# Performance work log

Measured on AMD Instinct MI355X. Metric: run time of the kernel, lower is better.

Reference implementation:

```python
import jax, jax.numpy as jnp
import numpy as np

H, C = 4, 32
NT, NDAT, NDEV = 50000, 20000, 4
EDT, EVT, ETT = 800000, 200000, 400000


def _gat_conv(xs, xd, src, dst, ea, Ws, Wd, We, As, Ad, Ae, b, n_dst, concat):
    # linear projections -> [N, H, C]
    hs = (xs @ Ws).reshape(-1, H, C)
    hd = (xd @ Wd).reshape(-1, H, C)
    he = (ea @ We).reshape(-1, H, C)
    # per-edge attention logits [E, H]
    al = (hs * As).sum(-1)[src] + (hd * Ad).sum(-1)[dst] + (he * Ae).sum(-1)
    al = jax.nn.leaky_relu(al, 0.2)
    # segment softmax over incoming edges of each dst node
    amax = jax.ops.segment_max(al, dst, num_segments=n_dst)
    amax = jnp.where(jnp.isfinite(amax), amax, 0.0)
    ex = jnp.exp(al - amax[dst])
    den = jax.ops.segment_sum(ex, dst, num_segments=n_dst)
    w = ex / (den[dst] + 1e-16)
    # weighted scatter-add of source messages
    out = jax.ops.segment_sum(hs[src] * w[..., None], dst, num_segments=n_dst)
    out = out.reshape(n_dst, H * C) if concat else out.mean(axis=1)
    return out + b


def _add_self_loops_mean(src, dst, ea, n):
    # PyG add_self_loops(fill_value='mean'): loop edge_attr = mean of incoming edge_attr per node
    cnt = jax.ops.segment_sum(jnp.ones(dst.shape, ea.dtype), dst, num_segments=n)
    ea_mean = jax.ops.segment_sum(ea, dst, num_segments=n) / jnp.maximum(cnt, 1.0)[:, None]
    loops = jnp.arange(n, dtype=src.dtype)
    return (jnp.concatenate([src, loops]), jnp.concatenate([dst, loops]),
            jnp.concatenate([ea, ea_mean], axis=0))


def setup_inputs() -> dict:
    key = jax.random.key(0)
    ks = iter(jax.random.split(key, 40))
    nrm = lambda shape, fan: jax.random.normal(next(ks), shape, jnp.float32) / np.sqrt(fan)
    inp = {}
    inp['x_data'] = jax.random.normal(next(ks), (NDAT, 8), jnp.float32)
    inp['x_tasks'] = jax.random.normal(next(ks), (NT, 16), jnp.float32)
    inp['x_dev'] = jax.random.normal(next(ks), (NDEV, 8), jnp.float32)
    inp['ei_dt'] = jnp.stack([jax.random.randint(next(ks), (EDT,), 0, NDAT),
                              jax.random.randint(next(ks), (EDT,), 0, NT)]).astype(jnp.int32)
    inp['ea_dt'] = jax.random.normal(next(ks), (EDT, 8), jnp.float32)
    inp['ei_vt'] = jnp.stack([jax.random.randint(next(ks), (EVT,), 0, NDEV),
                              jax.random.randint(next(ks), (EVT,), 0, NT)]).astype(jnp.int32)
    inp['ea_vt'] = jax.random.normal(next(ks), (EVT, 6), jnp.float32)
    inp['ei_tt'] = jnp.stack([jax.random.randint(next(ks), (ETT,), 0, NT),
                              jax.random.randint(next(ks), (ETT,), 0, NT)]).astype(jnp.int32)
    inp['ea_tt'] = jax.random.normal(next(ks), (ETT, 4), jnp.float32)
    # conv1: (data -> tasks), concat=True
    inp['Ws1'] = nrm((8, H * C), 8); inp['Wd1'] = nrm((16, H * C), 16); inp['We1'] = nrm((8, H * C), 8)
    inp['As1'] = nrm((H, C), C); inp['Ad1'] = nrm((H, C), C); inp['Ae1'] = nrm((H, C), C)
    inp['b1'] = jnp.zeros((H * C,), jnp.float32)
    # conv2: (devices -> tasks), concat=True
    inp['Ws2'] = nrm((8, H * C), 8); inp['Wd2'] = nrm((16, H * C), 16); inp['We2'] = nrm((6, H * C), 6)
    inp['As2'] = nrm((H, C), C); inp['Ad2'] = nrm((H, C), C); inp['Ae2'] = nrm((H, C), C)
    inp['b2'] = jnp.zeros((H * C,), jnp.float32)
    # conv3: tasks -> tasks, single lin (256 -> H*C), concat=False, self loops
    inp['W3'] = nrm((2 * H * C, H * C), 2 * H * C); inp['We3'] = nrm((4, H * C), 4)
    inp['As3'] = nrm((H, C), C); inp['Ad3'] = nrm((H, C), C); inp['Ae3'] = nrm((H, C), C)
    inp['b3'] = jnp.zeros((C,), jnp.float32)
    return inp


def reference(x_data, x_tasks, x_dev, ei_dt, ea_dt, ei_vt, ea_vt, ei_tt, ea_tt,
              Ws1, Wd1, We1, As1, Ad1, Ae1, b1,
              Ws2, Wd2, We2, As2, Ad2, Ae2, b2,
              W3, We3, As3, Ad3, Ae3, b3):
    t_data = jax.nn.relu(_gat_conv(x_data, x_tasks, ei_dt[0], ei_dt[1], ea_dt,
                                   Ws1, Wd1, We1, As1, Ad1, Ae1, b1, NT, True))
    t_dev = jax.nn.relu(_gat_conv(x_dev, x_tasks, ei_vt[0], ei_vt[1], ea_vt,
                                  Ws2, Wd2, We2, As2, Ad2, Ae2, b2, NT, True))
    tasks = jnp.concatenate([t_data, t_dev], axis=1)  # [NT, 256]
    src, dst, ea = _add_self_loops_mean(ei_tt[0], ei_tt[1], ea_tt, NT)
    x = _gat_conv(tasks, tasks, src, dst, ea, W3, W3, We3, As3, Ad3, Ae3, b3, NT, False)
    x = jax.nn.relu(x)
    # dropout(p=0.5) is identity in eval mode
    return x
```

## Files before the change

kernel.cpp:

```cpp
#include <hip/hip_runtime.h>
#include <math.h>

static const int NT = 50000, NDAT = 20000, NDEV = 4;
static const int EDT = 800000, EVT = 200000, ETT = 400000;

static const int SCAN_TILE = 2048, SCAN_NB = 25;

static const int HT   = EDT + EVT + ETT;
static const int IN_A = HT + NDAT * 128;
static const int IN_B = IN_A + NDAT * 4;
static const int IN_C = IN_B + NT * 4;
static const int IN_D = IN_C + NDEV * 128;
static const int IN_E = IN_D + NDEV * 4;
static const int IN_F = IN_E + 256 * 128;
static const int FRONT_N = IN_F;

static const size_t OFF_TASKS = 0;
static const size_t OFF_HS    = 12800000;
static const size_t OFF_RANK  = OFF_HS;
static const size_t OFF_HSB1  = OFF_HS + 1400000;
static const size_t OFF_REC1  = OFF_HS + 2680000;
static const size_t OFF_HSB3  = OFF_HS;
static const size_t OFF_REC2  = 19200000;
static const size_t OFF_REC3  = 20000000;
static const size_t OFF_DEG   = 23200000;
static const size_t OFF_RP    = 23350000;
static const size_t OFF_AS1   = 23500004;
static const size_t OFF_AD1   = 23580004;
static const size_t OFF_AD2   = 23780004;
static const size_t OFF_HS2   = 23980004;
static const size_t OFF_AS2   = 23980516;
static const size_t OFF_QS1   = 23980532;
static const size_t OFF_QD1   = 23980564;
static const size_t OFF_P1    = 23980628;
static const size_t OFF_QS2   = 23980660;
static const size_t OFF_QD2   = 23980692;
static const size_t OFF_P2    = 23980756;
static const size_t OFF_P3    = 23980780;
static const size_t OFF_BSUM  = 23980796;
static const size_t OFF_W3HT  = 23980924;
static const size_t OFF_W3LT  = 23997308;
static const size_t WS_TOTAL  = 24013692;

typedef short v8s __attribute__((ext_vector_type(8)));
typedef float v4f __attribute__((ext_vector_type(4)));

__device__ __forceinline__ float lrelu(float a) { return a > 0.f ? a : 0.2f * a; }
__device__ __forceinline__ unsigned short f2bf(float x) {
    unsigned int u = __float_as_uint(x);
    return (unsigned short)((u + 0x7FFFu + ((u >> 16) & 1u)) >> 16);
}
__device__ __forceinline__ float bf2f(unsigned short h) {
    return __uint_as_float(((unsigned int)h) << 16);
}
__device__ __forceinline__ float bfsel(unsigned int lo01, unsigned int lo23, int h) {
    unsigned int word = (h < 2) ? lo01 : lo23;
    return bf2f((unsigned short)((h & 1) ? (word >> 16) : (word & 0xFFFFu)));
}
__device__ __forceinline__ void cvt_split(const float4& A, const float4& B, v8s& hi, v8s& lo) {
    union { unsigned short u[8]; v8s v; } H, L;
    float f[8] = {A.x, A.y, A.z, A.w, B.x, B.y, B.z, B.w};
    #pragma unroll
    for (int i = 0; i < 8; ++i) {
        unsigned short h = f2bf(f[i]);
        H.u[i] = h;
        L.u[i] = f2bf(f[i] - bf2f(h));
    }
    hi = H.v; lo = L.v;
}

__global__ void k_proj_small(const float* Ws1, const float* As1,
                             const float* Wd1, const float* Ad1,
                             const float* We1, const float* Ae1,
                             const float* Ws2, const float* As2,
                             const float* Wd2, const float* Ad2,
                             const float* We2, const float* Ae2,
                             const float* We3, const float* Ae3,
                             float* Qs1, float* Qd1, float* P1,
                             float* Qs2, float* Qd2, float* P2, float* P3) {
    int t = threadIdx.x;
    const float *W, *A; float* O; int u;
    if      (t < 32)  { W = Ws1; A = As1; O = Qs1; u = t; }
    else if (t < 96)  { W = Wd1; A = Ad1; O = Qd1; u = t - 32; }
    else if (t < 128) { W = We1; A = Ae1; O = P1;  u = t - 96; }
    else if (t < 160) { W = Ws2; A = As2; O = Qs2; u = t - 128; }
    else if (t < 224) { W = Wd2; A = Ad2; O = Qd2; u = t - 160; }
    else if (t < 248) { W = We2; A = Ae2; O = P2;  u = t - 224; }
    else if (t < 264) { W = We3; A = Ae3; O = P3;  u = t - 248; }
    else return;
    int k = u >> 2, h = u & 3;
    float acc = 0.f;
    for (int c = 0; c < 32; ++c) acc += W[k * 128 + h * 32 + c] * A[h * 32 + c];
    O[k * 4 + h] = acc;
}

__global__ __launch_bounds__(256) void k_front(const float* __restrict__ x_data,
                                               const float* __restrict__ Ws1,
                                               unsigned short* __restrict__ hsb1,
                                               const float* __restrict__ Qs1,
                                               float* __restrict__ as1,
                                               const float* __restrict__ x_tasks,
                                               const float* __restrict__ Qd1,
                                               const float* __restrict__ Qd2,
                                               float* __restrict__ ad1, float* __restrict__ ad2,
                                               const float* __restrict__ x_dev,
                                               const float* __restrict__ Ws2,
                                               float* __restrict__ hs2,
                                               const float* __restrict__ Qs2,
                                               float* __restrict__ as2,
                                               const float* __restrict__ W3,
                                               unsigned short* __restrict__ w3hT,
                                               unsigned short* __restrict__ w3lT,
                                               const int* __restrict__ dt,
                                               const int* __restrict__ vt,
                                               const int* __restrict__ tt,
                                               int* __restrict__ deg,
                                               int* __restrict__ rank) {
    int idx = blockIdx.x * blockDim.x + threadIdx.x;
    if (idx < HT) {
        if (idx < EDT) {
            int d = dt[EDT + idx];
            int r = atomicAdd(&deg[d], 1);
            rank[idx] = (r << 16) | d;
        } else if (idx < EDT + EVT) {
            int d = vt[EVT + (idx - EDT)];
            int r = atomicAdd(&deg[NT + d], 1);
            rank[idx] = (r << 16) | d;
        } else {
            int d = tt[ETT + (idx - EDT - EVT)];
            int r = atomicAdd(&deg[2 * NT + d], 1);
            rank[idx] = (r << 16) | d;
        }
    } else if (idx < IN_A) {
        int i = idx - HT;
        int n = i >> 7, j = i & 127;
        float acc = 0.f;
        #pragma unroll
        for (int k = 0; k < 8; ++k) acc += x_data[n * 8 + k] * Ws1[k * 128 + j];
        hsb1[i] = f2bf(acc);
    } else if (idx < IN_B) {
        int i = idx - IN_A;
        int n = i >> 2, h = i & 3;
        float acc = 0.f;
        #pragma unroll
        for (int k = 0; k < 8; ++k) acc += x_data[n * 8 + k] * Qs1[k * 4 + h];
        as1[i] = acc;
    } else if (idx < IN_C) {
        int i = idx - IN_B;
        int n = i >> 2, h = i & 3;
        float a = 0.f, b = 0.f;
        #pragma unroll
        for (int k = 0; k < 16; ++k) {
            float v = x_tasks[n * 16 + k];
            a += v * Qd1[k * 4 + h];
            b += v * Qd2[k * 4 + h];
        }
        ad1[i] = a; ad2[i] = b;
    } else if (idx < IN_D) {
        int i = idx - IN_C;
        int n = i >> 7, j = i & 127;
        float acc = 0.f;
        #pragma unroll
        for (int k = 0; k < 8; ++k) acc += x_dev[n * 8 + k] * Ws2[k * 128 + j];
        hs2[i] = acc;
    } else if (idx < IN_E) {
        int i = idx - IN_D;
        int n = i >> 2, h = i & 3;
        float acc = 0.f;
        #pragma unroll
        for (int k = 0; k < 8; ++k) acc += x_dev[n * 8 + k] * Qs2[k * 4 + h];
        as2[i] = acc;
    } else if (idx < IN_F) {
        int i = idx - IN_E;
        int k = i >> 7, n = i & 127;
        float x = W3[i];
        unsigned short h = f2bf(x);
        w3hT[n * 256 + k] = h;
        w3lT[n * 256 + k] = f2bf(x - bf2f(h));
    }
}

__global__ __launch_bounds__(256) void k_scan_part(const int* __restrict__ deg,
                                                   int* __restrict__ bsum) {
    int b = blockIdx.x;
    int g = b / SCAN_NB, t = b % SCAN_NB;
    int base = t * SCAN_TILE + threadIdx.x * 8;
    const int* dg = deg + (size_t)g * NT;
    int s = 0;
    if (base + 8 <= NT) {
        int4 a = *reinterpret_cast<const int4*>(dg + base);
        int4 c = *reinterpret_cast<const int4*>(dg + base + 4);
        s = a.x + a.y + a.z + a.w + c.x + c.y + c.z + c.w;
    } else {
        for (int i = 0; i < 8; ++i) if (base + i < NT) s += dg[base + i];
    }
    __shared__ int red[256];
    red[threadIdx.x] = s;
    __syncthreads();
    for (int off = 128; off > 0; off >>= 1) {
        if (threadIdx.x < off) red[threadIdx.x] += red[threadIdx.x + off];
        __syncthreads();
    }
    if (threadIdx.x == 0) bsum[b] = red[0];
}

__global__ __launch_bounds__(256) void k_scan_final(const int* __restrict__ deg,
                                                    const int* __restrict__ bsum,
                                                    int* __restrict__ rp) {
    int b = blockIdx.x;
    int g = b / SCAN_NB, t = b % SCAN_NB;
    int tid = threadIdx.x;
    int base = t * SCAN_TILE + tid * 8;
    const int* dg = deg + (size_t)g * NT;
    int* rpg = rp + (size_t)g * (NT + 1);
    int v[8];
    int s = 0;
    if (base + 8 <= NT) {
        int4 a = *reinterpret_cast<const int4*>(dg + base);
        int4 c = *reinterpret_cast<const int4*>(dg + base + 4);
        v[0] = a.x; v[1] = a.y; v[2] = a.z; v[3] = a.w;
        v[4] = c.x; v[5] = c.y; v[6] = c.z; v[7] = c.w;
        s = v[0] + v[1] + v[2] + v[3] + v[4] + v[5] + v[6] + v[7];
    } else {
        #pragma unroll
        for (int i = 0; i < 8; ++i) {
            v[i] = (base + i < NT) ? dg[base + i] : 0;
            s += v[i];
        }
    }
    __shared__ int sums[256];
    sums[tid] = s;
    __syncthreads();
    for (int off = 1; off < 256; off <<= 1) {
        int x = (tid >= off) ? sums[tid - off] : 0;
        __syncthreads();
        sums[tid] += x;
        __syncthreads();
    }
    int toff = 0;
    for (int t2 = 0; t2 < t; ++t2) toff += bsum[g * SCAN_NB + t2];
    int run = toff + (tid ? sums[tid - 1] : 0);
    #pragma unroll
    for (int i = 0; i < 8; ++i) {
        int idx = base + i;
        if (idx < NT) {
            rpg[idx] = run; run += v[i];
            if (idx == NT - 1) rpg[NT] = run;
        }
    }
}

__global__ void k_permute_w(const int* __restrict__ dt, const int* __restrict__ vt,
                            const int* __restrict__ tt, const int* __restrict__ rank,
                            const int* __restrict__ rp,
                            const float* __restrict__ as1, const float* __restrict__ ad1,
                            const float* __restrict__ P1, const float* __restrict__ ea1,
                            const float* __restrict__ as2, const float* __restrict__ ad2,
                            const float* __restrict__ P2, const float* __restrict__ ea2,
                            const float* __restrict__ P3, const float* __restrict__ ea3,
                            uint4* __restrict__ rec1, uint4* __restrict__ rec2,
                            uint4* __restrict__ rec3) {
    int e = blockIdx.x * blockDim.x + threadIdx.x;
    if (e < EDT) {
        int rk = rank[e];
        int d = rk & 0xFFFF;
        int s = dt[e];
        int slot = rp[d] + (rk >> 16);
        float l[4];
        #pragma unroll
        for (int h = 0; h < 4; ++h) l[h] = as1[s * 4 + h] + ad1[d * 4 + h];
        float4 A = *reinterpret_cast<const float4*>(&ea1[(size_t)e * 8]);
        float4 B = *reinterpret_cast<const float4*>(&ea1[(size_t)e * 8 + 4]);
        float ev[8] = {A.x, A.y, A.z, A.w, B.x, B.y, B.z, B.w};
        #pragma unroll
        for (int k = 0; k < 8; ++k)
            #pragma unroll
            for (int h = 0; h < 4; ++h) l[h] += ev[k] * P1[k * 4 + h];
        unsigned int w01 = (unsigned int)f2bf(expf(lrelu(l[0])))
                         | ((unsigned int)f2bf(expf(lrelu(l[1]))) << 16);
        unsigned int w23 = (unsigned int)f2bf(expf(lrelu(l[2])))
                         | ((unsigned int)f2bf(expf(lrelu(l[3]))) << 16);
        rec1[slot] = make_uint4(w01, w23, (unsigned int)s, 0u);
    } else if (e < EDT + EVT) {
        int ee = e - EDT;
        int rk = rank[e];
        int d = rk & 0xFFFF;
        int s = vt[ee];
        int slot = rp[(NT + 1) + d] + (rk >> 16);
        float l[4];
        #pragma unroll
        for (int h = 0; h < 4; ++h) l[h] = as2[s * 4 + h] + ad2[d * 4 + h];
        float2 a = *reinterpret_cast<const float2*>(&ea2[(size_t)ee * 6]);
        float2 b = *reinterpret_cast<const float2*>(&ea2[(size_t)ee * 6 + 2]);
        float2 c = *reinterpret_cast<const float2*>(&ea2[(size_t)ee * 6 + 4]);
        float ev[6] = {a.x, a.y, b.x, b.y, c.x, c.y};
        #pragma unroll
        for (int k = 0; k < 6; ++k)
            #pragma unroll
            for (int h = 0; h < 4; ++h) l[h] += ev[k] * P2[k * 4 + h];
        unsigned int w01 = (unsigned int)f2bf(expf(lrelu(l[0])))
                         | ((unsigned int)f2bf(expf(lrelu(l[1]))) << 16);
        unsigned int w23 = (unsigned int)f2bf(expf(lrelu(l[2])))
                         | ((unsigned int)f2bf(expf(lrelu(l[3]))) << 16);
        rec2[slot] = make_uint4(w01, w23, (unsigned int)s, 0u);
    } else if (e < EDT + EVT + ETT) {
        int ee = e - EDT - EVT;
        int rk = rank[e];
        int d = rk & 0xFFFF;
        int s = tt[ee];
        int slot = rp[2 * (NT + 1) + d] + (rk >> 16);
        float4 q = *reinterpret_cast<const float4*>(&ea3[(size_t)ee * 4]);
        float ae[4];
        #pragma unroll
        for (int h = 0; h < 4; ++h)
            ae[h] = q.x * P3[h] + q.y * P3[4 + h] + q.z * P3[8 + h] + q.w * P3[12 + h];
        unsigned int a01 = (unsigned int)f2bf(ae[0]) | ((unsigned int)f2bf(ae[1]) << 16);
        unsigned int a23 = (unsigned int)f2bf(ae[2]) | ((unsigned int)f2bf(ae[3]) << 16);
        rec3[slot] = make_uint4((unsigned int)s, a01, a23, 0u);
    }
}

__global__ __launch_bounds__(256) void k_gather12(const int* __restrict__ rp1,
                                                  const uint4* __restrict__ rec1,
                                                  const unsigned short* __restrict__ hsb,
                                                  const float* __restrict__ b1,
                                                  const int* __restrict__ rp2,
                                                  const uint4* __restrict__ rec2,
                                                  const float* __restrict__ hs2,
                                                  const float* __restrict__ b2,
                                                  float* __restrict__ tasks) {
    int tid = threadIdx.x;
    int lane = tid & 31;
    int h = lane >> 3;
    if (blockIdx.x < NT / 8) {
        int d = blockIdx.x * 8 + (tid >> 5);
        int c0 = (lane & 7) * 4;
        int i0 = rp1[d], i1 = rp1[d + 1];
        float a0 = 0.f, a1 = 0.f, a2 = 0.f, a3 = 0.f, den = 0.f;
        int i = i0;
        for (; i + 4 <= i1; i += 4) {
            uint4 r0 = rec1[i], r1 = rec1[i + 1], r2 = rec1[i + 2], r3 = rec1[i + 3];
            float w0 = bfsel(r0.x, r0.y, h);
            float w1 = bfsel(r1.x, r1.y, h);
            float w2 = bfsel(r2.x, r2.y, h);
            float w3 = bfsel(r3.x, r3.y, h);
            ushort4 m0 = *reinterpret_cast<const ushort4*>(&hsb[(size_t)r0.z * 128 + h * 32 + c0]);
            ushort4 m1 = *reinterpret_cast<const ushort4*>(&hsb[(size_t)r1.z * 128 + h * 32 + c0]);
            ushort4 m2 = *reinterpret_cast<const ushort4*>(&hsb[(size_t)r2.z * 128 + h * 32 + c0]);
            ushort4 m3 = *reinterpret_cast<const ushort4*>(&hsb[(size_t)r3.z * 128 + h * 32 + c0]);
            a0 += w0 * bf2f(m0.x) + w1 * bf2f(m1.x) + w2 * bf2f(m2.x) + w3 * bf2f(m3.x);
            a1 += w0 * bf2f(m0.y) + w1 * bf2f(m1.y) + w2 * bf2f(m2.y) + w3 * bf2f(m3.y);
            a2 += w0 * bf2f(m0.z) + w1 * bf2f(m1.z) + w2 * bf2f(m2.z) + w3 * bf2f(m3.z);
            a3 += w0 * bf2f(m0.w) + w1 * bf2f(m1.w) + w2 * bf2f(m2.w) + w3 * bf2f(m3.w);
            den += w0 + w1 + w2 + w3;
        }
        for (; i < i1; ++i) {
            uint4 r = rec1[i];
            float w = bfsel(r.x, r.y, h);
            ushort4 m = *reinterpret_cast<const ushort4*>(&hsb[(size_t)r.z * 128 + h * 32 + c0]);
            a0 += w * bf2f(m.x); a1 += w * bf2f(m.y);
            a2 += w * bf2f(m.z); a3 += w * bf2f(m.w);
            den += w;
        }
        int j0 = h * 32 + c0;
        float4 b4 = *reinterpret_cast<const float4*>(&b1[j0]);
        float r = 1.f / (den + 1e-16f);
        float4 o = make_float4(fmaxf(a0 * r + b4.x, 0.f), fmaxf(a1 * r + b4.y, 0.f),
                               fmaxf(a2 * r + b4.z, 0.f), fmaxf(a3 * r + b4.w, 0.f));
        *reinterpret_cast<float4*>(&tasks[(size_t)d * 256 + j0]) = o;
    } else {
        int d = (blockIdx.x - NT / 8) * 8 + (tid >> 5);
        int i0 = rp2[d], i1 = rp2[d + 1];
        float ax = 0.f, ay = 0.f, az = 0.f, aw = 0.f, den = 0.f;
        int i = i0;
        for (; i + 4 <= i1; i += 4) {
            uint4 r0 = rec2[i], r1 = rec2[i + 1], r2 = rec2[i + 2], r3 = rec2[i + 3];
            float w0 = bfsel(r0.x, r0.y, h);
            float w1 = bfsel(r1.x, r1.y, h);
            float w2 = bfsel(r2.x, r2.y, h);
            float w3 = bfsel(r3.x, r3.y, h);
            float4 v0 = *reinterpret_cast<const float4*>(&hs2[r0.z * 128 + lane * 4]);
            float4 v1 = *reinterpret_cast<const float4*>(&hs2[r1.z * 128 + lane * 4]);
            float4 v2 = *reinterpret_cast<const float4*>(&hs2[r2.z * 128 + lane * 4]);
            float4 v3 = *reinterpret_cast<const float4*>(&hs2[r3.z * 128 + lane * 4]);
            ax += v0.x * w0 + v1.x * w1 + v2.x * w2 + v3.x * w3;
            ay += v0.y * w0 + v1.y * w1 + v2.y * w2 + v3.y * w3;
            az += v0.z * w0 + v1.z * w1 + v2.z * w2 + v3.z * w3;
            aw += v0.w * w0 + v1.w * w1 + v2.w * w2 + v3.w * w3;
            den += w0 + w1 + w2 + w3;
        }
        for (; i < i1; ++i) {
            uint4 r4 = rec2[i];
            float w = bfsel(r4.x, r4.y, h);
            float4 v = *reinterpret_cast<const float4*>(&hs2[r4.z * 128 + lane * 4]);
            ax += v.x * w; ay += v.y * w; az += v.z * w; aw += v.w * w;
            den += w;
        }
        float4 b4 = *reinterpret_cast<const float4*>(&b2[lane * 4]);
        float r = 1.f / (den + 1e-16f);
        float4 o = make_float4(fmaxf(ax * r + b4.x, 0.f), fmaxf(ay * r + b4.y, 0.f),
                               fmaxf(az * r + b4.z, 0.f), fmaxf(aw * r + b4.w, 0.f));
        *reinterpret_cast<float4*>(&tasks[(size_t)d * 256 + 128 + lane * 4]) = o;
    }
}

__global__ __launch_bounds__(256) void k_gather_c3(const int* __restrict__ rp,
                                                   const uint4* __restrict__ rec,
                                                   const float* __restrict__ as3,
                                                   const float* __restrict__ ad3,
                                                   const unsigned short* __restrict__ hsb,
                                                   const float* __restrict__ b3,
                                                   float* __restrict__ out) {
    int tid = threadIdx.x;
    int d = blockIdx.x * 8 + (tid >> 5);
    int lane = tid & 31;
    int h = lane >> 3;
    int c0 = (lane & 7) * 4;
    float adv = ad3[d * 4 + h];
    int i0 = rp[d], i1 = rp[d + 1];
    float a0 = 0.f, a1 = 0.f, a2 = 0.f, a3 = 0.f, den = 0.f, aes = 0.f;
    int i = i0;
    for (; i + 4 <= i1; i += 4) {
        uint4 r0 = rec[i], r1 = rec[i + 1], r2 = rec[i + 2], r3 = rec[i + 3];
        float s0 = as3[(size_t)r0.x * 4 + h], s1 = as3[(size_t)r1.x * 4 + h];
        float s2 = as3[(size_t)r2.x * 4 + h], s3 = as3[(size_t)r3.x * 4 + h];
        ushort4 m0 = *reinterpret_cast<const ushort4*>(&hsb[(size_t)r0.x * 128 + h * 32 + c0]);
        ushort4 m1 = *reinterpret_cast<const ushort4*>(&hsb[(size_t)r1.x * 128 + h * 32 + c0]);
        ushort4 m2 = *reinterpret_cast<const ushort4*>(&hsb[(size_t)r2.x * 128 + h * 32 + c0]);
        ushort4 m3 = *reinterpret_cast<const ushort4*>(&hsb[(size_t)r3.x * 128 + h * 32 + c0]);
        float ae0 = bfsel(r0.y, r0.z, h);
        float ae1 = bfsel(r1.y, r1.z, h);
        float ae2 = bfsel(r2.y, r2.z, h);
        float ae3 = bfsel(r3.y, r3.z, h);
        float w0 = expf(lrelu(s0 + adv + ae0));
        float w1 = expf(lrelu(s1 + adv + ae1));
        float w2 = expf(lrelu(s2 + adv + ae2));
        float w3 = expf(lrelu(s3 + adv + ae3));
        a0 += w0 * bf2f(m0.x) + w1 * bf2f(m1.x) + w2 * bf2f(m2.x) + w3 * bf2f(m3.x);
        a1 += w0 * bf2f(m0.y) + w1 * bf2f(m1.y) + w2 * bf2f(m2.y) + w3 * bf2f(m3.y);
        a2 += w0 * bf2f(m0.z) + w1 * bf2f(m1.z) + w2 * bf2f(m2.z) + w3 * bf2f(m3.z);
        a3 += w0 * bf2f(m0.w) + w1 * bf2f(m1.w) + w2 * bf2f(m2.w) + w3 * bf2f(m3.w);
        den += w0 + w1 + w2 + w3;
        aes += ae0 + ae1 + ae2 + ae3;
    }
    for (; i < i1; ++i) {
        uint4 r4 = rec[i];
        float s = as3[(size_t)r4.x * 4 + h];
        ushort4 m = *reinterpret_cast<const ushort4*>(&hsb[(size_t)r4.x * 128 + h * 32 + c0]);
        float ae = bfsel(r4.y, r4.z, h);
        float w = expf(lrelu(s + adv + ae));
        a0 += w * bf2f(m.x); a1 += w * bf2f(m.y);
        a2 += w * bf2f(m.z); a3 += w * bf2f(m.w);
        den += w; aes += ae;
    }
    float cnt = (float)(i1 - i0);
    float mloop = aes / fmaxf(cnt, 1.f);
    float exl = expf(lrelu(as3[(size_t)d * 4 + h] + adv + mloop));
    ushort4 md = *reinterpret_cast<const ushort4*>(&hsb[(size_t)d * 128 + h * 32 + c0]);
    float rden = 1.f / (den + exl + 1e-16f);
    float p0 = (a0 + exl * bf2f(md.x)) * rden;
    float p1 = (a1 + exl * bf2f(md.y)) * rden;
    float p2 = (a2 + exl * bf2f(md.z)) * rden;
    float p3 = (a3 + exl * bf2f(md.w)) * rden;
    p0 += __shfl_xor(p0, 8, 32); p0 += __shfl_xor(p0, 16, 32);
    p1 += __shfl_xor(p1, 8, 32); p1 += __shfl_xor(p1, 16, 32);
    p2 += __shfl_xor(p2, 8, 32); p2 += __shfl_xor(p2, 16, 32);
    p3 += __shfl_xor(p3, 8, 32); p3 += __shfl_xor(p3, 16, 32);
    if ((lane >> 3) == 0) {
        float4 o;
        o.x = fmaxf(0.25f * p0 + b3[c0 + 0], 0.f);
        o.y = fmaxf(0.25f * p1 + b3[c0 + 1], 0.f);
        o.z = fmaxf(0.25f * p2 + b3[c0 + 2], 0.f);
        o.w = fmaxf(0.25f * p3 + b3[c0 + 3], 0.f);
        *reinterpret_cast<float4*>(&out[(size_t)d * 32 + c0]) = o;
    }
}

__global__ __launch_bounds__(256, 2) void k_gemm_mfma(const float* __restrict__ T,
                                                      const unsigned short* __restrict__ w3hT,
                                                      const unsigned short* __restrict__ w3lT,
                                                      const float* __restrict__ As3,
                                                      const float* __restrict__ Ad3,
                                                      unsigned short* __restrict__ hsb,
                                                      float* __restrict__ as3o,
                                                      float* __restrict__ ad3o) {
    __shared__ uint4 sB[2][2048];
    int tid = threadIdx.x;
    int lane = tid & 63;
    int arow = lane & 15;
    int kgrp = lane >> 4;
    int s0 = blockIdx.x * 8 + (tid >> 6) * 2;
    int ss0 = s0 < 3125 ? s0 : 3124;
    int ss1 = (s0 + 1) < 3125 ? (s0 + 1) : 3124;
    const uint4* w3h4 = reinterpret_cast<const uint4*>(w3hT);
    const uint4* w3l4 = reinterpret_cast<const uint4*>(w3lT);

    v4f acc[2][8];
    #pragma unroll
    for (int sp = 0; sp < 2; ++sp)
        #pragma unroll
        for (int nt = 0; nt < 8; ++nt) acc[sp][nt] = (v4f)0.f;

    #pragma unroll
    for (int kt = 0; kt < 2; ++kt) {
        __syncthreads();
        float4 a0[8], a1[8];
        const float* Ta0 = T + (size_t)(ss0 * 16 + arow) * 256 + kt * 128 + kgrp * 8;
        const float* Ta1 = T + (size_t)(ss1 * 16 + arow) * 256 + kt * 128 + kgrp * 8;
        #pragma unroll
        for (int kc = 0; kc < 4; ++kc) {
            a0[kc * 2]     = *reinterpret_cast<const float4*>(Ta0 + kc * 32);
            a0[kc * 2 + 1] = *reinterpret_cast<const float4*>(Ta0 + kc * 32 + 4);
            a1[kc * 2]     = *reinterpret_cast<const float4*>(Ta1 + kc * 32);
            a1[kc * 2 + 1] = *reinterpret_cast<const float4*>(Ta1 + kc * 32 + 4);
        }
        #pragma unroll
        for (int it = 0; it < 8; ++it) {
            int c = it * 256 + tid;
            int n = c >> 4, ch = c & 15;
            int gi = n * 32 + kt * 16 + ch;
            int li = n * 16 + (ch ^ (n & 7));
            sB[0][li] = w3h4[gi];
            sB[1][li] = w3l4[gi];
        }
        __syncthreads();
        #pragma unroll
        for (int kc = 0; kc < 4; ++kc) {
            v8s ah0, al0, ah1, al1;
            cvt_split(a0[kc * 2], a0[kc * 2 + 1], ah0, al0);
            cvt_split(a1[kc * 2], a1[kc * 2 + 1], ah1, al1);
            #pragma unroll
            for (int nt = 0; nt < 8; ++nt) {
                int col = nt * 16 + arow;
                int ch = kc * 4 + kgrp;
                int li = col * 16 + (ch ^ (col & 7));
                v8s bh = *reinterpret_cast<const v8s*>(&sB[0][li]);
                v8s bl = *reinterpret_cast<const v8s*>(&sB[1][li]);
                acc[0][nt] = __builtin_amdgcn_mfma_f32_16x16x32_bf16(ah0, bh, acc[0][nt], 0, 0, 0);
                acc[0][nt] = __builtin_amdgcn_mfma_f32_16x16x32_bf16(ah0, bl, acc[0][nt], 0, 0, 0);
                acc[0][nt] = __builtin_amdgcn_mfma_f32_16x16x32_bf16(al0, bh, acc[0][nt], 0, 0, 0);
                acc[1][nt] = __builtin_amdgcn_mfma_f32_16x16x32_bf16(ah1, bh, acc[1][nt], 0, 0, 0);
                acc[1][nt] = __builtin_amdgcn_mfma_f32_16x16x32_bf16(ah1, bl, acc[1][nt], 0, 0, 0);
                acc[1][nt] = __builtin_amdgcn_mfma_f32_16x16x32_bf16(al1, bh, acc[1][nt], 0, 0, 0);
            }
        }
    }
    float As3v[8], Ad3v[8];
    #pragma unroll
    for (int nt = 0; nt < 8; ++nt) {
        As3v[nt] = As3[nt * 16 + arow];
        Ad3v[nt] = Ad3[nt * 16 + arow];
    }
    #pragma unroll
    for (int sp = 0; sp < 2; ++sp) {
        int s = s0 + sp;
        if (s >= 3125) continue;
        #pragma unroll
        for (int i = 0; i < 4; ++i) {
            int row = s * 16 + kgrp * 4 + i;
            #pragma unroll
            for (int nt = 0; nt < 8; ++nt)
                hsb[(size_t)row * 128 + nt * 16 + arow] = f2bf(acc[sp][nt][i]);
            #pragma unroll
            for (int h = 0; h < 4; ++h) {
                float pa = acc[sp][2 * h][i] * As3v[2 * h] + acc[sp][2 * h + 1][i] * As3v[2 * h + 1];
                float pb = acc[sp][2 * h][i] * Ad3v[2 * h] + acc[sp][2 * h + 1][i] * Ad3v[2 * h + 1];
                #pragma unroll
                for (int off = 1; off < 16; off <<= 1) {
                    pa += __shfl_xor(pa, off, 64);
                    pb += __shfl_xor(pb, off, 64);
                }
                if (arow == 0) {
                    as3o[row * 4 + h] = pa;
                    ad3o[row * 4 + h] = pb;
                }
            }
        }
    }
}

extern "C" void kernel_launch(void* const* d_in, const int* in_sizes, int n_in,
                              void* d_out, int out_size, void* d_ws, size_t ws_size,
                              hipStream_t stream) {
    const float* x_data  = (const float*)d_in[0];
    const float* x_tasks = (const float*)d_in[1];
    const float* x_dev   = (const float*)d_in[2];
    const int*   ei_dt   = (const int*)d_in[3];
    const float* ea_dt   = (const float*)d_in[4];
    const int*   ei_vt   = (const int*)d_in[5];
    const float* ea_vt   = (const float*)d_in[6];
    const int*   ei_tt   = (const int*)d_in[7];
    const float* ea_tt   = (const float*)d_in[8];
    const float* Ws1 = (const float*)d_in[9];  const float* Wd1 = (const float*)d_in[10];
    const float* We1 = (const float*)d_in[11]; const float* As1 = (const float*)d_in[12];
    const float* Ad1 = (const float*)d_in[13]; const float* Ae1 = (const float*)d_in[14];
    const float* b1  = (const float*)d_in[15];
    const float* Ws2 = (const float*)d_in[16]; const float* Wd2 = (const float*)d_in[17];
    const float* We2 = (const float*)d_in[18]; const float* As2 = (const float*)d_in[19];
    const float* Ad2 = (const float*)d_in[20]; const float* Ae2 = (const float*)d_in[21];
    const float* b2  = (const float*)d_in[22];
    const float* W3  = (const float*)d_in[23]; const float* We3 = (const float*)d_in[24];
    const float* As3 = (const float*)d_in[25]; const float* Ad3 = (const float*)d_in[26];
    const float* Ae3 = (const float*)d_in[27]; const float* b3  = (const float*)d_in[28];

    if (ws_size < WS_TOTAL * sizeof(float)) return;

    float* w = (float*)d_ws;
    float* tasks = w + OFF_TASKS;
    int*   rank  = (int*)(w + OFF_RANK);
    unsigned short* hsb1 = (unsigned short*)(w + OFF_HSB1);
    unsigned short* hsb3 = (unsigned short*)(w + OFF_HSB3);
    uint4* rec1  = (uint4*)(w + OFF_REC1);
    uint4* rec2  = (uint4*)(w + OFF_REC2);
    uint4* rec3  = (uint4*)(w + OFF_REC3);
    int*   deg   = (int*)(w + OFF_DEG);
    int*   rp    = (int*)(w + OFF_RP);
    int*   bsum  = (int*)(w + OFF_BSUM);
    unsigned short* w3hT = (unsigned short*)(w + OFF_W3HT);
    unsigned short* w3lT = (unsigned short*)(w + OFF_W3LT);
    float* as1 = w + OFF_AS1;
    float* ad1 = w + OFF_AD1; float* as3 = w + OFF_AD1;
    float* ad2 = w + OFF_AD2; float* ad3 = w + OFF_AD2;
    float* hs2 = w + OFF_HS2; float* as2 = w + OFF_AS2;
    float* Qs1 = w + OFF_QS1; float* Qd1 = w + OFF_QD1; float* P1 = w + OFF_P1;
    float* Qs2 = w + OFF_QS2; float* Qd2 = w + OFF_QD2; float* P2 = w + OFF_P2;
    float* P3  = w + OFF_P3;
    float* out = (float*)d_out;

    dim3 B(256);
    #define GRID(n) dim3((unsigned)(((n) + 255) / 256))

    hipMemsetAsync(deg, 0, 3 * NT * sizeof(int), stream);
    k_proj_small<<<1, 320, 0, stream>>>(Ws1, As1, Wd1, Ad1, We1, Ae1,
                                        Ws2, As2, Wd2, Ad2, We2, Ae2, We3, Ae3,
                                        Qs1, Qd1, P1, Qs2, Qd2, P2, P3);
    k_front<<<GRID(FRONT_N), B, 0, stream>>>(x_data, Ws1, hsb1, Qs1, as1,
                                             x_tasks, Qd1, Qd2, ad1, ad2,
                                             x_dev, Ws2, hs2, Qs2, as2,
                                             W3, w3hT, w3lT,
                                             ei_dt, ei_vt, ei_tt, deg, rank);
    k_scan_part<<<dim3(3 * SCAN_NB), B, 0, stream>>>(deg, bsum);
    k_scan_final<<<dim3(3 * SCAN_NB), B, 0, stream>>>(deg, bsum, rp);
    k_permute_w<<<GRID(EDT + EVT + ETT), B, 0, stream>>>(ei_dt, ei_vt, ei_tt, rank, rp,
                                                         as1, ad1, P1, ea_dt,
                                                         as2, ad2, P2, ea_vt,
                                                         P3, ea_tt,
                                                         rec1, rec2, rec3);
    k_gather12<<<dim3(2 * (NT / 8)), B, 0, stream>>>(rp, rec1, hsb1, b1,
                                                     rp + (NT + 1), rec2, hs2, b2, tasks);
    k_gemm_mfma<<<dim3(391), dim3(256), 0, stream>>>(tasks, w3hT, w3lT, As3, Ad3,
                                                     hsb3, as3, ad3);
    k_gather_c3<<<dim3(NT / 8), B, 0, stream>>>(rp + 2 * (NT + 1), rec3, as3, ad3,
                                                hsb3, b3, out);
    #undef GRID
}
```

Before: 213.7 us.

## Recompute conv1 source projection on the fly in gather instead of materializing

Stops precomputing the bf16 x_data@Ws1 table (20000x128) in k_front. k_gather12 now keeps each lane's 8x4 slice of Ws1 in registers and rebuilds the message from the 8-float x_data row of every edge. Each edge gathers 32 bytes of raw features instead of a 256-byte projected row, and the front kernel loses 2.56M threads of work. In exchange every edge costs about 32 extra FMAs per lane. Because messages are now computed in fp32 rather than rounded to bf16, precision improves slightly.

```diff
diff --git a/kernel.cpp b/kernel.cpp
--- a/kernel.cpp
+++ b/kernel.cpp
@@ -7,8 +7,7 @@
 static const int SCAN_TILE = 2048, SCAN_NB = 25;
 
 static const int HT   = EDT + EVT + ETT;
-static const int IN_A = HT + NDAT * 128;
-static const int IN_B = IN_A + NDAT * 4;
+static const int IN_B = HT + NDAT * 4;
 static const int IN_C = IN_B + NT * 4;
 static const int IN_D = IN_C + NDEV * 128;
 static const int IN_E = IN_D + NDEV * 4;
@@ -18,7 +17,6 @@
 static const size_t OFF_TASKS = 0;
 static const size_t OFF_HS    = 12800000;
 static const size_t OFF_RANK  = OFF_HS;
-static const size_t OFF_HSB1  = OFF_HS + 1400000;
 static const size_t OFF_REC1  = OFF_HS + 2680000;
 static const size_t OFF_HSB3  = OFF_HS;
 static const size_t OFF_REC2  = 19200000;
@@ -95,8 +93,6 @@
 }
 
 __global__ __launch_bounds__(256) void k_front(const float* __restrict__ x_data,
-                                               const float* __restrict__ Ws1,
-                                               unsigned short* __restrict__ hsb1,
                                                const float* __restrict__ Qs1,
                                                float* __restrict__ as1,
                                                const float* __restrict__ x_tasks,
@@ -131,15 +127,8 @@
             int r = atomicAdd(&deg[2 * NT + d], 1);
             rank[idx] = (r << 16) | d;
         }
-    } else if (idx < IN_A) {
+    } else if (idx < IN_B) {
         int i = idx - HT;
-        int n = i >> 7, j = i & 127;
-        float acc = 0.f;
-        #pragma unroll
-        for (int k = 0; k < 8; ++k) acc += x_data[n * 8 + k] * Ws1[k * 128 + j];
-        hsb1[i] = f2bf(acc);
-    } else if (idx < IN_B) {
-        int i = idx - IN_A;
         int n = i >> 2, h = i & 3;
         float acc = 0.f;
         #pragma unroll
@@ -322,7 +311,8 @@
 
 __global__ __launch_bounds__(256) void k_gather12(const int* __restrict__ rp1,
                                                   const uint4* __restrict__ rec1,
-                                                  const unsigned short* __restrict__ hsb,
+                                                  const float* __restrict__ xd,
+                                                  const float* __restrict__ Ws1,
                                                   const float* __restrict__ b1,
                                                   const int* __restrict__ rp2,
                                                   const uint4* __restrict__ rec2,
@@ -334,7 +324,10 @@
     int h = lane >> 3;
     if (blockIdx.x < NT / 8) {
         int d = blockIdx.x * 8 + (tid >> 5);
-        int c0 = (lane & 7) * 4;
+        float4 Wc[8];
+        #pragma unroll
+        for (int k = 0; k < 8; ++k)
+            Wc[k] = *reinterpret_cast<const float4*>(&Ws1[k * 128 + lane * 4]);
         int i0 = rp1[d], i1 = rp1[d + 1];
         float a0 = 0.f, a1 = 0.f, a2 = 0.f, a3 = 0.f, den = 0.f;
         int i = i0;
@@ -344,25 +337,71 @@
             float w1 = bfsel(r1.x, r1.y, h);
             float w2 = bfsel(r2.x, r2.y, h);
             float w3 = bfsel(r3.x, r3.y, h);
-            ushort4 m0 = *reinterpret_cast<const ushort4*>(&hsb[(size_t)r0.z * 128 + h * 32 + c0]);
-            ushort4 m1 = *reinterpret_cast<const ushort4*>(&hsb[(size_t)r1.z * 128 + h * 32 + c0]);
-            ushort4 m2 = *reinterpret_cast<const ushort4*>(&hsb[(size_t)r2.z * 128 + h * 32 + c0]);
-            ushort4 m3 = *reinterpret_cast<const ushort4*>(&hsb[(size_t)r3.z * 128 + h * 32 + c0]);
-            a0 += w0 * bf2f(m0.x) + w1 * bf2f(m1.x) + w2 * bf2f(m2.x) + w3 * bf2f(m3.x);
-            a1 += w0 * bf2f(m0.y) + w1 * bf2f(m1.y) + w2 * bf2f(m2.y) + w3 * bf2f(m3.y);
-            a2 += w0 * bf2f(m0.z) + w1 * bf2f(m1.z) + w2 * bf2f(m2.z) + w3 * bf2f(m3.z);
-            a3 += w0 * bf2f(m0.w) + w1 * bf2f(m1.w) + w2 * bf2f(m2.w) + w3 * bf2f(m3.w);
+            float4 xa0 = *reinterpret_cast<const float4*>(&xd[(size_t)r0.z * 8]);
+            float4 xb0 = *reinterpret_cast<const float4*>(&xd[(size_t)r0.z * 8 + 4]);
+            float4 xa1 = *reinterpret_cast<const float4*>(&xd[(size_t)r1.z * 8]);
+            float4 xb1 = *reinterpret_cast<const float4*>(&xd[(size_t)r1.z * 8 + 4]);
+            float4 xa2 = *reinterpret_cast<const float4*>(&xd[(size_t)r2.z * 8]);
+            float4 xb2 = *reinterpret_cast<const float4*>(&xd[(size_t)r2.z * 8 + 4]);
+            float4 xa3 = *reinterpret_cast<const float4*>(&xd[(size_t)r3.z * 8]);
+            float4 xb3 = *reinterpret_cast<const float4*>(&xd[(size_t)r3.z * 8 + 4]);
+            float4 m0, m1, m2, m3;
+            m0.x = xa0.x*Wc[0].x + xa0.y*Wc[1].x + xa0.z*Wc[2].x + xa0.w*Wc[3].x
+                 + xb0.x*Wc[4].x + xb0.y*Wc[5].x + xb0.z*Wc[6].x + xb0.w*Wc[7].x;
+            m0.y = xa0.x*Wc[0].y + xa0.y*Wc[1].y + xa0.z*Wc[2].y + xa0.w*Wc[3].y
+                 + xb0.x*Wc[4].y + xb0.y*Wc[5].y + xb0.z*Wc[6].y + xb0.w*Wc[7].y;
+            m0.z = xa0.x*Wc[0].z + xa0.y*Wc[1].z + xa0.z*Wc[2].z + xa0.w*Wc[3].z
+                 + xb0.x*Wc[4].z + xb0.y*Wc[5].z + xb0.z*Wc[6].z + xb0.w*Wc[7].z;
+            m0.w = xa0.x*Wc[0].w + xa0.y*Wc[1].w + xa0.z*Wc[2].w + xa0.w*Wc[3].w
+                 + xb0.x*Wc[4].w + xb0.y*Wc[5].w + xb0.z*Wc[6].w + xb0.w*Wc[7].w;
+            m1.x = xa1.x*Wc[0].x + xa1.y*Wc[1].x + xa1.z*Wc[2].x + xa1.w*Wc[3].x
+                 + xb1.x*Wc[4].x + xb1.y*Wc[5].x + xb1.z*Wc[6].x + xb1.w*Wc[7].x;
+            m1.y = xa1.x*Wc[0].y + xa1.y*Wc[1].y + xa1.z*Wc[2].y + xa1.w*Wc[3].y
+                 + xb1.x*Wc[4].y + xb1.y*Wc[5].y + xb1.z*Wc[6].y + xb1.w*Wc[7].y;
+            m1.z = xa1.x*Wc[0].z + xa1.y*Wc[1].z + xa1.z*Wc[2].z + xa1.w*Wc[3].z
+                 + xb1.x*Wc[4].z + xb1.y*Wc[5].z + xb1.z*Wc[6].z + xb1.w*Wc[7].z;
+            m1.w = xa1.x*Wc[0].w + xa1.y*Wc[1].w + xa1.z*Wc[2].w + xa1.w*Wc[3].w
+                 + xb1.x*Wc[4].w + xb1.y*Wc[5].w + xb1.z*Wc[6].w + xb1.w*Wc[7].w;
+            m2.x = xa2.x*Wc[0].x + xa2.y*Wc[1].x + xa2.z*Wc[2].x + xa2.w*Wc[3].x
+                 + xb2.x*Wc[4].x + xb2.y*Wc[5].x + xb2.z*Wc[6].x + xb2.w*Wc[7].x;
+            m2.y = xa2.x*Wc[0].y + xa2.y*Wc[1].y + xa2.z*Wc[2].y + xa2.w*Wc[3].y
+                 + xb2.x*Wc[4].y + xb2.y*Wc[5].y + xb2.z*Wc[6].y + xb2.w*Wc[7].y;
+            m2.z = xa2.x*Wc[0].z + xa2.y*Wc[1].z + xa2.z*Wc[2].z + xa2.w*Wc[3].z
+                 + xb2.x*Wc[4].z + xb2.y*Wc[5].z + xb2.z*Wc[6].z + xb2.w*Wc[7].z;
+            m2.w = xa2.x*Wc[0].w + xa2.y*Wc[1].w + xa2.z*Wc[2].w + xa2.w*Wc[3].w
+                 + xb2.x*Wc[4].w + xb2.y*Wc[5].w + xb2.z*Wc[6].w + xb2.w*Wc[7].w;
+            m3.x = xa3.x*Wc[0].x + xa3.y*Wc[1].x + xa3.z*Wc[2].x + xa3.w*Wc[3].x
+                 + xb3.x*Wc[4].x + xb3.y*Wc[5].x + xb3.z*Wc[6].x + xb3.w*Wc[7].x;
+            m3.y = xa3.x*Wc[0].y + xa3.y*Wc[1].y + xa3.z*Wc[2].y + xa3.w*Wc[3].y
+                 + xb3.x*Wc[4].y + xb3.y*Wc[5].y + xb3.z*Wc[6].y + xb3.w*Wc[7].y;
+            m3.z = xa3.x*Wc[0].z + xa3.y*Wc[1].z + xa3.z*Wc[2].z + xa3.w*Wc[3].z
+                 + xb3.x*Wc[4].z + xb3.y*Wc[5].z + xb3.z*Wc[6].z + xb3.w*Wc[7].z;
+            m3.w = xa3.x*Wc[0].w + xa3.y*Wc[1].w + xa3.z*Wc[2].w + xa3.w*Wc[3].w
+                 + xb3.x*Wc[4].w + xb3.y*Wc[5].w + xb3.z*Wc[6].w + xb3.w*Wc[7].w;
+            a0 += w0 * m0.x + w1 * m1.x + w2 * m2.x + w3 * m3.x;
+            a1 += w0 * m0.y + w1 * m1.y + w2 * m2.y + w3 * m3.y;
+            a2 += w0 * m0.z + w1 * m1.z + w2 * m2.z + w3 * m3.z;
+            a3 += w0 * m0.w + w1 * m1.w + w2 * m2.w + w3 * m3.w;
             den += w0 + w1 + w2 + w3;
         }
         for (; i < i1; ++i) {
             uint4 r = rec1[i];
             float w = bfsel(r.x, r.y, h);
-            ushort4 m = *reinterpret_cast<const ushort4*>(&hsb[(size_t)r.z * 128 + h * 32 + c0]);
-            a0 += w * bf2f(m.x); a1 += w * bf2f(m.y);
-            a2 += w * bf2f(m.z); a3 += w * bf2f(m.w);
+            float4 xa = *reinterpret_cast<const float4*>(&xd[(size_t)r.z * 8]);
+            float4 xb = *reinterpret_cast<const float4*>(&xd[(size_t)r.z * 8 + 4]);
+            float4 m;
+            m.x = xa.x*Wc[0].x + xa.y*Wc[1].x + xa.z*Wc[2].x + xa.w*Wc[3].x
+                + xb.x*Wc[4].x + xb.y*Wc[5].x + xb.z*Wc[6].x + xb.w*Wc[7].x;
+            m.y = xa.x*Wc[0].y + xa.y*Wc[1].y + xa.z*Wc[2].y + xa.w*Wc[3].y
+                + xb.x*Wc[4].y + xb.y*Wc[5].y + xb.z*Wc[6].y + xb.w*Wc[7].y;
+            m.z = xa.x*Wc[0].z + xa.y*Wc[1].z + xa.z*Wc[2].z + xa.w*Wc[3].z
+                + xb.x*Wc[4].z + xb.y*Wc[5].z + xb.z*Wc[6].z + xb.w*Wc[7].z;
+            m.w = xa.x*Wc[0].w + xa.y*Wc[1].w + xa.z*Wc[2].w + xa.w*Wc[3].w
+                + xb.x*Wc[4].w + xb.y*Wc[5].w + xb.z*Wc[6].w + xb.w*Wc[7].w;
+            a0 += w * m.x; a1 += w * m.y; a2 += w * m.z; a3 += w * m.w;
             den += w;
         }
-        int j0 = h * 32 + c0;
+        int j0 = lane * 4;
         float4 b4 = *reinterpret_cast<const float4*>(&b1[j0]);
         float r = 1.f / (den + 1e-16f);
         float4 o = make_float4(fmaxf(a0 * r + b4.x, 0.f), fmaxf(a1 * r + b4.y, 0.f),
@@ -608,7 +647,6 @@
     float* w = (float*)d_ws;
     float* tasks = w + OFF_TASKS;
     int*   rank  = (int*)(w + OFF_RANK);
-    unsigned short* hsb1 = (unsigned short*)(w + OFF_HSB1);
     unsigned short* hsb3 = (unsigned short*)(w + OFF_HSB3);
     uint4* rec1  = (uint4*)(w + OFF_REC1);
     uint4* rec2  = (uint4*)(w + OFF_REC2);
@@ -634,7 +672,7 @@
     k_proj_small<<<1, 320, 0, stream>>>(Ws1, As1, Wd1, Ad1, We1, Ae1,
                                         Ws2, As2, Wd2, Ad2, We2, Ae2, We3, Ae3,
                                         Qs1, Qd1, P1, Qs2, Qd2, P2, P3);
-    k_front<<<GRID(FRONT_N), B, 0, stream>>>(x_data, Ws1, hsb1, Qs1, as1,
+    k_front<<<GRID(FRONT_N), B, 0, stream>>>(x_data, Qs1, as1,
                                              x_tasks, Qd1, Qd2, ad1, ad2,
                                              x_dev, Ws2, hs2, Qs2, as2,
                                              W3, w3hT, w3lT,
@@ -646,7 +684,7 @@
                                                          as2, ad2, P2, ea_vt,
                                                          P3, ea_tt,
                                                          rec1, rec2, rec3);
-    k_gather12<<<dim3(2 * (NT / 8)), B, 0, stream>>>(rp, rec1, hsb1, b1,
+    k_gather12<<<dim3(2 * (NT / 8)), B, 0, stream>>>(rp, rec1, x_data, Ws1, b1,
                                                      rp + (NT + 1), rec2, hs2, b2, tasks);
     k_gemm_mfma<<<dim3(391), dim3(256), 0, stream>>>(tasks, w3hT, w3lT, As3, Ad3,
                                                      hsb3, as3, ad3);
```

Result: slower. 250.5 us (+17.2%).
